# Optimization experiments

Hardware: AMD Instinct MI355X
Metric: run time of the kernel (lower is better)

The kernel has to match this reference:

```python
import jax, jax.numpy as jnp
import numpy as np

N_NODES = 50000
N_EDGES = 800000
NFEAT, NHID, NOUT = 128, 128, 64


def _glorot(key, shape):
    lim = 1.0 / np.sqrt(shape[0])
    return jax.random.uniform(key, shape, jnp.float32, -lim, lim)


def setup_inputs() -> dict:
    key = jax.random.key(0)
    ks = jax.random.split(key, 12)
    x = jax.random.normal(ks[0], (N_NODES, NFEAT), jnp.float32)
    edge_src = jax.random.randint(ks[1], (N_EDGES,), 0, N_NODES, jnp.int32)
    edge_dst = jax.random.randint(ks[2], (N_EDGES,), 0, N_NODES, jnp.int32)
    edge_w = jax.random.uniform(ks[3], (N_EDGES,), jnp.float32)  # normalized adj values
    # layer params: nfeat->nhid, nhid->nhid, nhid->nhid, nhid->nout
    W0, b0 = _glorot(ks[4], (NFEAT, NHID)), jnp.zeros((NHID,), jnp.float32)
    W1, b1 = _glorot(ks[5], (NHID, NHID)), jnp.zeros((NHID,), jnp.float32)
    W2, b2 = _glorot(ks[6], (NHID, NHID)), jnp.zeros((NHID,), jnp.float32)
    W3, b3 = _glorot(ks[7], (NHID, NOUT)), jnp.zeros((NOUT,), jnp.float32)
    return dict(x=x, edge_src=edge_src, edge_dst=edge_dst, edge_w=edge_w,
                W0=W0, b0=b0, W1=W1, b1=b1, W2=W2, b2=b2, W3=W3, b3=b3)


def _gcn_layer(h, src, dst, w, W, b):
    # support = h @ W ; out = A @ support + b  (A given as weighted edge list)
    support = h @ W                               # [N, d_out]
    msgs = support[src] * w[:, None]              # [E, d_out] gather + scale
    agg = jax.ops.segment_sum(msgs, dst, num_segments=N_NODES)  # scatter-add
    return agg + b


def reference(x, edge_src, edge_dst, edge_w, W0, b0, W1, b1, W2, b2, W3, b3):
    # eval mode: dropout is identity
    h = jax.nn.relu(_gcn_layer(x, edge_src, edge_dst, edge_w, W0, b0))
    h = jax.nn.relu(_gcn_layer(h, edge_src, edge_dst, edge_w, W1, b1))
    h = jax.nn.relu(_gcn_layer(h, edge_src, edge_dst, edge_w, W2, b2))
    h = _gcn_layer(h, edge_src, edge_dst, edge_w, W3, b3)  # no relu on last layer
    return h
```

## Files before the change

kernel.cpp:

```cpp
#include <hip/hip_runtime.h>


constexpr int NN = 50000;
constexpr int NE = 800000;
constexpr int NB = (NN + 127) >> 7;
constexpr int CAP = 4608;
constexpr int PART_CHUNK = 4096;
constexpr int PART_GRID = (NE + PART_CHUNK - 1) / PART_CHUNK;
constexpr int ZOFF = NB * CAP;

typedef __attribute__((ext_vector_type(8))) short bf16x8;
typedef __attribute__((ext_vector_type(4))) float floatx4;
typedef __attribute__((ext_vector_type(2))) float floatx2;
typedef __attribute__((ext_vector_type(4))) unsigned int uintx4;

__device__ inline unsigned short f2bf(float f) {
    unsigned u = __float_as_uint(f);
    u += 0x7fffu + ((u >> 16) & 1u);
    return (unsigned short)(u >> 16);
}
__device__ inline float bflo(unsigned v) { return __uint_as_float(v << 16); }
__device__ inline float bfhi(unsigned v) { return __uint_as_float(v & 0xffff0000u); }
__device__ inline unsigned char f2fp8(float f) {
    return (unsigned char)(__builtin_amdgcn_cvt_pk_fp8_f32(f, f, 0, false) & 0xff);
}


__global__ void k_prep(
        const float* __restrict__ W0, const float* __restrict__ W1,
        const float* __restrict__ W2, const float* __restrict__ W3,
        unsigned short* __restrict__ T0, unsigned short* __restrict__ T1,
        unsigned short* __restrict__ T2, unsigned short* __restrict__ T3,
        int* __restrict__ bfill, unsigned* __restrict__ es) {
    int b = blockIdx.x;
    if (b == 448) {
        for (int i = threadIdx.x; i < NB; i += 128) bfill[i] = 0;
        if (threadIdx.x < 16) es[ZOFF + threadIdx.x] = 0u;
        return;
    }
    const float* W; unsigned short* T; int N, n;
    if (b < 128)      { W = W0; T = T0; N = 128; n = b; }
    else if (b < 256) { W = W1; T = T1; N = 128; n = b - 128; }
    else if (b < 384) { W = W2; T = T2; N = 128; n = b - 256; }
    else              { W = W3; T = T3; N = 64;  n = b - 384; }
    int k = threadIdx.x;
    T[n * 128 + k] = f2bf(W[(size_t)k * N + n]);
}


__device__ inline bf16x8 ldA_f32(const float* A, size_t off) {
    float4 u = *(const float4*)&A[off];
    float4 v = *(const float4*)&A[off + 4];
    bf16x8 r;
    r[0] = (short)f2bf(u.x); r[1] = (short)f2bf(u.y);
    r[2] = (short)f2bf(u.z); r[3] = (short)f2bf(u.w);
    r[4] = (short)f2bf(v.x); r[5] = (short)f2bf(v.y);
    r[6] = (short)f2bf(v.z); r[7] = (short)f2bf(v.w);
    return r;
}

__global__ __launch_bounds__(256) void k_pg0(
        const int* __restrict__ src, const int* __restrict__ dst,
        const float* __restrict__ w, int* __restrict__ bfill,
        int2* __restrict__ ep,
        const float* __restrict__ A,
        const unsigned short* __restrict__ Wt,
        unsigned char* __restrict__ C,
        int M) {
    __shared__ int hist[NB], base[NB], off[NB];
    __shared__ unsigned short sWt[128 * 136];

    const int tid = threadIdx.x;

    if (blockIdx.x < PART_GRID) {
        for (int b = tid; b < NB; b += 256) { hist[b] = 0; off[b] = 0; }
        __syncthreads();

        int e0 = blockIdx.x * PART_CHUNK;
        int  sreg[16]; int wreg[16]; short breg[16];
#pragma unroll
        for (int i = 0; i < 16; ++i) {
            int e = e0 + i * 256 + tid;
            if (e < NE) {
                int d = dst[e];
                int b = d >> 7;
                sreg[i] = (src[e] & 0xffff) | ((d & 127) << 16);
                wreg[i] = __float_as_int(w[e]);
                breg[i] = (short)b;
                atomicAdd(&hist[b], 1);
            } else breg[i] = -1;
        }
        __syncthreads();
        for (int b = tid; b < NB; b += 256)
            base[b] = b * CAP + atomicAdd(&bfill[b], hist[b]);
        __syncthreads();
#pragma unroll
        for (int i = 0; i < 16; ++i) {
            if (breg[i] >= 0) {
                int b = breg[i];
                int p = atomicAdd(&off[b], 1);
                ep[base[b] + p] = make_int2(sreg[i], wreg[i]);
            }
        }
        return;
    }

    constexpr int STR = 136;
    const int gb = blockIdx.x - PART_GRID;
#pragma unroll
    for (int i = 0; i < 8; ++i) {
        int c = i * 256 + tid;
        int row = c >> 4, col = (c & 15) * 8;
        *(uint4*)&sWt[row * STR + col] = *(const uint4*)&Wt[row * 128 + col];
    }

    const int wv = tid >> 6;
    const int ln = tid & 63;
    const int m  = ln & 15;
    const int qd = ln >> 4;

    int gr  = gb * 64 + wv * 16 + m;
    int grc = (gr < M) ? gr : (M - 1);
    bf16x8 af[4];
#pragma unroll
    for (int s = 0; s < 4; ++s)
        af[s] = ldA_f32(A, (size_t)grc * 128 + s * 32 + qd * 8);

    __syncthreads();

    floatx4 acc[8];
#pragma unroll
    for (int c = 0; c < 8; ++c) {
        acc[c] = (floatx4){0.f, 0.f, 0.f, 0.f};
#pragma unroll
        for (int s = 0; s < 4; ++s) {
            bf16x8 bf = *(const bf16x8*)&sWt[(c * 16 + m) * STR + s * 32 + qd * 8];
            acc[c] = __builtin_amdgcn_mfma_f32_16x16x32_bf16(af[s], bf, acc[c], 0, 0, 0);
        }
    }

    int row0 = gb * 64 + wv * 16 + qd * 4;
#pragma unroll
    for (int c = 0; c < 8; ++c)
#pragma unroll
        for (int r = 0; r < 4; ++r) {
            int row = row0 + r;
            if (row < M) C[(size_t)row * 128 + c * 16 + m] = f2fp8(acc[c][r]);
        }
}

__global__ __launch_bounds__(256) void k_sort(
        const int2* __restrict__ ep, const int* __restrict__ bfill,
        unsigned* __restrict__ es, int2* __restrict__ begend) {
    __shared__ int cnt[128], base[128], fl[128];
    __shared__ int s_total;
    int b  = blockIdx.x;
    int n0 = b << 7;
    int nn = min(128, NN - n0);
    int t  = threadIdx.x;
    if (t < 128) { cnt[t] = 0; fl[t] = 0; }
    __syncthreads();
    int bbase = b * CAP;
    int beg = bbase, end = bbase + bfill[b];
    for (int e = beg + t; e < end; e += 256)
        atomicAdd(&cnt[(ep[e].x >> 16) & 127], 1);
    __syncthreads();
    int cp = (t < 128) ? ((cnt[t] + 15) & ~15) : 0;
    if (t < 128) base[t] = cp;
    __syncthreads();
    for (int off = 1; off < 128; off <<= 1) {
        int add = (t >= off && t < 128) ? base[t - off] : 0;
        __syncthreads();
        if (t < 128) base[t] += add;
        __syncthreads();
    }
    if (t == 127) s_total = base[127];
    __syncthreads();
    int total = s_total;
    for (int i = t; i < total + 16; i += 256) es[bbase + i] = 0u;
    if (t < nn) {
        int off = base[t] - cp;
        begend[n0 + t] = make_int2(bbase + off, bbase + off + cp);
    }
    __syncthreads();
    for (int e = beg + t; e < end; e += 256) {
        int2 v = ep[e];
        int d = (v.x >> 16) & 127;
        int off = base[d] - ((cnt[d] + 15) & ~15);
        int pos = bbase + off + atomicAdd(&fl[d], 1);
        es[pos] = (unsigned)(v.x & 0xffff) |
                  ((unsigned)f2bf(__int_as_float(v.y)) << 16);
    }
}


#define FMAP8(W, R)                                                             \
    { floatx2 p0 = __builtin_amdgcn_cvt_pk_f32_fp8((int)(R).x, false);          \
      floatx2 p1 = __builtin_amdgcn_cvt_pk_f32_fp8((int)(R).x, true);           \
      floatx2 p2 = __builtin_amdgcn_cvt_pk_f32_fp8((int)(R).y, false);          \
      floatx2 p3 = __builtin_amdgcn_cvt_pk_f32_fp8((int)(R).y, true);           \
      acc[0] = fmaf(W, p0.x, acc[0]); acc[1] = fmaf(W, p0.y, acc[1]);           \
      acc[2] = fmaf(W, p1.x, acc[2]); acc[3] = fmaf(W, p1.y, acc[3]);           \
      acc[4] = fmaf(W, p2.x, acc[4]); acc[5] = fmaf(W, p2.y, acc[5]);           \
      acc[6] = fmaf(W, p3.x, acc[6]); acc[7] = fmaf(W, p3.y, acc[7]); }

#define GATHF(R, MV)                                                            \
    uint2 R = *(const uint2*)&sup[(size_t)((MV) & 0xffffu) * 128 + l * 8];

template<int NOUT, typename CT>
__global__ __launch_bounds__(256) void k_fused(
        const unsigned char* __restrict__ sup,
        const int2* __restrict__ begend, const unsigned* __restrict__ es,
        const float* __restrict__ bias,
        const unsigned short* __restrict__ Wt,
        CT* __restrict__ C,
        int M) {
    constexpr int NT  = NOUT / 16;
    constexpr int STR = 136;
    __shared__ unsigned short hT[16 * STR];

    const int tid = threadIdx.x;
    const int l   = tid & 15;
    const int n0  = blockIdx.x * 16;
    const int n   = n0 + (tid >> 4);
    const bool nv = n < NN;

    int2 be = nv ? begend[n] : make_int2(0, 0);
    const int en = be.y;
    int e = be.x;
    float acc[8] = {0.f, 0.f, 0.f, 0.f, 0.f, 0.f, 0.f, 0.f};
    bool v = e < en;
    if (__any(v)) {
        int ei = v ? e : ZOFF;
        uintx4 m0 = __builtin_nontemporal_load((const uintx4*)&es[ei]);
        uintx4 m1 = __builtin_nontemporal_load((const uintx4*)&es[ei + 4]);
        for (;;) {
            GATHF(r0, m0[0]); GATHF(r1, m0[1]); GATHF(r2, m0[2]); GATHF(r3, m0[3]);
            GATHF(r4, m1[0]); GATHF(r5, m1[1]); GATHF(r6, m1[2]); GATHF(r7, m1[3]);
            float w0 = bfhi(m0[0]), w1 = bfhi(m0[1]), w2 = bfhi(m0[2]), w3 = bfhi(m0[3]);
            float w4 = bfhi(m1[0]), w5 = bfhi(m1[1]), w6 = bfhi(m1[2]), w7 = bfhi(m1[3]);
            e += 8;
            v = e < en;
            bool more = __any(v);
            int eo = v ? e : ZOFF;
            uintx4 p0 = __builtin_nontemporal_load((const uintx4*)&es[eo]);
            uintx4 p1 = __builtin_nontemporal_load((const uintx4*)&es[eo + 4]);
            FMAP8(w0, r0); FMAP8(w1, r1); FMAP8(w2, r2); FMAP8(w3, r3);
            FMAP8(w4, r4); FMAP8(w5, r5); FMAP8(w6, r6); FMAP8(w7, r7);
            m0 = p0; m1 = p1;
            if (!more) break;
        }
    }
    {
        uintx4 pk;
#pragma unroll
        for (int q = 0; q < 4; ++q) {
            float a0 = fmaxf(acc[2 * q]     + bias[l * 8 + 2 * q],     0.f);
            float a1 = fmaxf(acc[2 * q + 1] + bias[l * 8 + 2 * q + 1], 0.f);
            pk[q] = (unsigned)f2bf(a0) | ((unsigned)f2bf(a1) << 16);
        }
        *(uintx4*)&hT[(tid >> 4) * STR + l * 8] = pk;
    }
    __syncthreads();

    const int wv = tid >> 6;
    const int ln = tid & 63;
    const int m_ = ln & 15, qd = ln >> 4;
    const int c0 = wv * (NT / 4);
    bf16x8 af[4];
#pragma unroll
    for (int s = 0; s < 4; ++s)
        af[s] = *(const bf16x8*)&hT[m_ * STR + s * 32 + qd * 8];

    floatx4 acc2[NT / 4];
#pragma unroll
    for (int c = 0; c < NT / 4; ++c) {
        acc2[c] = (floatx4){0.f, 0.f, 0.f, 0.f};
#pragma unroll
        for (int s = 0; s < 4; ++s) {
            bf16x8 bf = *(const bf16x8*)&Wt[(size_t)((c0 + c) * 16 + m_) * 128 + s * 32 + qd * 8];
            acc2[c] = __builtin_amdgcn_mfma_f32_16x16x32_bf16(af[s], bf, acc2[c], 0, 0, 0);
        }
    }
    int row0 = n0 + qd * 4;
#pragma unroll
    for (int c = 0; c < NT / 4; ++c)
#pragma unroll
        for (int r = 0; r < 4; ++r) {
            int row = row0 + r;
            if (row < M) {
                if constexpr (sizeof(CT) == 1)
                    C[(size_t)row * NOUT + (c0 + c) * 16 + m_] = (CT)f2fp8(acc2[c][r]);
                else
                    C[(size_t)row * NOUT + (c0 + c) * 16 + m_] = (CT)f2bf(acc2[c][r]);
            }
        }
}


#define FMA4(W, R)                                                              \
    acc[0] = fmaf(W, bflo((R).x), acc[0]); acc[1] = fmaf(W, bfhi((R).x), acc[1]); \
    acc[2] = fmaf(W, bflo((R).y), acc[2]); acc[3] = fmaf(W, bfhi((R).y), acc[3]);

#define GATHO(R, MV)                                                            \
    uint2 R = *(const uint2*)&sup[(size_t)((MV) & 0xffffu) * 64 + l * 4];

__global__ __launch_bounds__(256) void k_agg64(
        const unsigned short* __restrict__ sup,
        const int2* __restrict__ begend, const unsigned* __restrict__ es,
        const float* __restrict__ bias, float* __restrict__ out) {
    const int tid = threadIdx.x;
    const int l   = tid & 15;
    const int n   = blockIdx.x * 16 + (tid >> 4);
    const bool nv = n < NN;

    int2 be = nv ? begend[n] : make_int2(0, 0);
    const int en = be.y;
    int e = be.x;
    float acc[4] = {0.f, 0.f, 0.f, 0.f};
    bool v = e < en;
    if (__any(v)) {
        int ei = v ? e : ZOFF;
        uintx4 m0 = __builtin_nontemporal_load((const uintx4*)&es[ei]);
        uintx4 m1 = __builtin_nontemporal_load((const uintx4*)&es[ei + 4]);
        for (;;) {
            GATHO(r0, m0[0]); GATHO(r1, m0[1]); GATHO(r2, m0[2]); GATHO(r3, m0[3]);
            GATHO(r4, m1[0]); GATHO(r5, m1[1]); GATHO(r6, m1[2]); GATHO(r7, m1[3]);
            float w0 = bfhi(m0[0]), w1 = bfhi(m0[1]), w2 = bfhi(m0[2]), w3 = bfhi(m0[3]);
            float w4 = bfhi(m1[0]), w5 = bfhi(m1[1]), w6 = bfhi(m1[2]), w7 = bfhi(m1[3]);
            e += 8;
            v = e < en;
            bool more = __any(v);
            int eo = v ? e : ZOFF;
            uintx4 p0 = __builtin_nontemporal_load((const uintx4*)&es[eo]);
            uintx4 p1 = __builtin_nontemporal_load((const uintx4*)&es[eo + 4]);
            FMA4(w0, r0); FMA4(w1, r1); FMA4(w2, r2); FMA4(w3, r3);
            FMA4(w4, r4); FMA4(w5, r5); FMA4(w6, r6); FMA4(w7, r7);
            m0 = p0; m1 = p1;
            if (!more) break;
        }
    }
    if (nv) {
        float4 o = make_float4(acc[0] + bias[l * 4],     acc[1] + bias[l * 4 + 1],
                               acc[2] + bias[l * 4 + 2], acc[3] + bias[l * 4 + 3]);
        *(float4*)&out[(size_t)n * 64 + l * 4] = o;
    }
}


extern "C" void kernel_launch(void* const* d_in, const int* in_sizes, int n_in,
                              void* d_out, int out_size, void* d_ws, size_t ws_size,
                              hipStream_t stream) {
    (void)in_sizes; (void)n_in; (void)out_size; (void)ws_size;

    const float* x    = (const float*)d_in[0];
    const int*   esrc = (const int*)d_in[1];
    const int*   edst = (const int*)d_in[2];
    const float* ew   = (const float*)d_in[3];
    const float* W0   = (const float*)d_in[4];
    const float* b0   = (const float*)d_in[5];
    const float* W1   = (const float*)d_in[6];
    const float* b1   = (const float*)d_in[7];
    const float* W2   = (const float*)d_in[8];
    const float* b2   = (const float*)d_in[9];
    const float* W3   = (const float*)d_in[10];
    const float* b3   = (const float*)d_in[11];

    char* p = (char*)d_ws;
    auto alloc = [&](size_t bytes) {
        char* r = p;
        p += (bytes + 511) & ~size_t(511);
        return r;
    };
    int*      bfill  = (int*)     alloc((size_t)NB * 4);
    int2*     begend = (int2*)    alloc((size_t)NN * 8);
    int2*     ep     = (int2*)    alloc((size_t)NB * CAP * 8);
    unsigned* es     = (unsigned*)alloc(((size_t)NB * CAP + 64) * 4);
    unsigned char*  s8a = (unsigned char*) alloc((size_t)NN * 128);
    unsigned char*  s8b = (unsigned char*) alloc((size_t)NN * 128);
    unsigned short* s16 = (unsigned short*)alloc((size_t)NN * 64 * 2);
    unsigned short* Wt0 = (unsigned short*)alloc((size_t)128 * 128 * 2);
    unsigned short* Wt1 = (unsigned short*)alloc((size_t)128 * 128 * 2);
    unsigned short* Wt2 = (unsigned short*)alloc((size_t)128 * 128 * 2);
    unsigned short* Wt3 = (unsigned short*)alloc((size_t)64 * 128 * 2);

    const int g_gemm = (NN + 63) / 64;
    const int f_grid = (NN + 15) / 16;

    k_prep<<<449, 128, 0, stream>>>(W0, W1, W2, W3, Wt0, Wt1, Wt2, Wt3,
                                    bfill, es);
    k_pg0<<<PART_GRID + g_gemm, 256, 0, stream>>>(
        esrc, edst, ew, bfill, ep, x, Wt0, s8a, NN);
    k_sort<<<NB, 256, 0, stream>>>(ep, bfill, es, begend);

    k_fused<128, unsigned char><<<f_grid, 256, 0, stream>>>(s8a, begend, es, b0, Wt1, s8b, NN);
    k_fused<128, unsigned char><<<f_grid, 256, 0, stream>>>(s8b, begend, es, b1, Wt2, s8a, NN);
    k_fused<64, unsigned short><<<f_grid, 256, 0, stream>>>(s8a, begend, es, b2, Wt3, s16, NN);
    k_agg64<<<f_grid, 256, 0, stream>>>(s16, begend, es, b3, (float*)d_out);
}
```

Before: 233.6 us.

## Merge weight prep with edge partition and sort with first GEMM

Restructures the preprocessing pipeline. The weight transpose/convert work is folded into the edge-partition kernel. The per-bucket sort is folded into the same launch as the first-layer GEMM. The zeroing of bfill and the es tail moves to hipMemsetAsync calls. This cuts kernel launches from three to two plus two memsets, and lets the sort and GEMM work overlap in one grid, at the cost of shared-memory aliasing between roles and two extra memset operations.

```diff
diff --git a/kernel.cpp b/kernel.cpp
--- a/kernel.cpp
+++ b/kernel.cpp
@@ -8,6 +8,7 @@
 constexpr int PART_CHUNK = 4096;
 constexpr int PART_GRID = (NE + PART_CHUNK - 1) / PART_CHUNK;
 constexpr int ZOFF = NB * CAP;
+constexpr int PREP_GRID = 224;
 
 typedef __attribute__((ext_vector_type(8))) short bf16x8;
 typedef __attribute__((ext_vector_type(4))) float floatx4;
@@ -26,25 +27,58 @@
 }
 
 
-__global__ void k_prep(
+__global__ __launch_bounds__(256) void k_pp(
         const float* __restrict__ W0, const float* __restrict__ W1,
         const float* __restrict__ W2, const float* __restrict__ W3,
         unsigned short* __restrict__ T0, unsigned short* __restrict__ T1,
         unsigned short* __restrict__ T2, unsigned short* __restrict__ T3,
-        int* __restrict__ bfill, unsigned* __restrict__ es) {
-    int b = blockIdx.x;
-    if (b == 448) {
-        for (int i = threadIdx.x; i < NB; i += 128) bfill[i] = 0;
-        if (threadIdx.x < 16) es[ZOFF + threadIdx.x] = 0u;
+        const int* __restrict__ src, const int* __restrict__ dst,
+        const float* __restrict__ w, int* __restrict__ bfill,
+        int2* __restrict__ ep) {
+    const int tid = threadIdx.x;
+
+    if (blockIdx.x < PREP_GRID) {
+        int r = blockIdx.x * 2 + (tid >> 7);
+        int k = tid & 127;
+        const float* W; unsigned short* T; int N, n;
+        if (r < 128)      { W = W0; T = T0; N = 128; n = r; }
+        else if (r < 256) { W = W1; T = T1; N = 128; n = r - 128; }
+        else if (r < 384) { W = W2; T = T2; N = 128; n = r - 256; }
+        else              { W = W3; T = T3; N = 64;  n = r - 384; }
+        T[n * 128 + k] = f2bf(W[(size_t)k * N + n]);
         return;
     }
-    const float* W; unsigned short* T; int N, n;
-    if (b < 128)      { W = W0; T = T0; N = 128; n = b; }
-    else if (b < 256) { W = W1; T = T1; N = 128; n = b - 128; }
-    else if (b < 384) { W = W2; T = T2; N = 128; n = b - 256; }
-    else              { W = W3; T = T3; N = 64;  n = b - 384; }
-    int k = threadIdx.x;
-    T[n * 128 + k] = f2bf(W[(size_t)k * N + n]);
+
+    __shared__ int hist[NB], base[NB], off[NB];
+    for (int b = tid; b < NB; b += 256) { hist[b] = 0; off[b] = 0; }
+    __syncthreads();
+
+    int e0 = (blockIdx.x - PREP_GRID) * PART_CHUNK;
+    int  sreg[16]; int wreg[16]; short breg[16];
+#pragma unroll
+    for (int i = 0; i < 16; ++i) {
+        int e = e0 + i * 256 + tid;
+        if (e < NE) {
+            int d = dst[e];
+            int b = d >> 7;
+            sreg[i] = (src[e] & 0xffff) | ((d & 127) << 16);
+            wreg[i] = __float_as_int(w[e]);
+            breg[i] = (short)b;
+            atomicAdd(&hist[b], 1);
+        } else breg[i] = -1;
+    }
+    __syncthreads();
+    for (int b = tid; b < NB; b += 256)
+        base[b] = b * CAP + atomicAdd(&bfill[b], hist[b]);
+    __syncthreads();
+#pragma unroll
+    for (int i = 0; i < 16; ++i) {
+        if (breg[i] >= 0) {
+            int b = breg[i];
+            int p = atomicAdd(&off[b], 1);
+            ep[base[b] + p] = make_int2(sreg[i], wreg[i]);
+        }
+    }
 }
 
 
@@ -59,54 +93,64 @@
     return r;
 }
 
-__global__ __launch_bounds__(256) void k_pg0(
-        const int* __restrict__ src, const int* __restrict__ dst,
-        const float* __restrict__ w, int* __restrict__ bfill,
-        int2* __restrict__ ep,
+__global__ __launch_bounds__(256) void k_sg(
+        const int2* __restrict__ ep, const int* __restrict__ bfill,
+        unsigned* __restrict__ es, int2* __restrict__ begend,
         const float* __restrict__ A,
         const unsigned short* __restrict__ Wt,
         unsigned char* __restrict__ C,
         int M) {
-    __shared__ int hist[NB], base[NB], off[NB];
-    __shared__ unsigned short sWt[128 * 136];
-
+    constexpr int STR = 136;
+    __shared__ int smem[128 * STR / 2];
     const int tid = threadIdx.x;
 
-    if (blockIdx.x < PART_GRID) {
-        for (int b = tid; b < NB; b += 256) { hist[b] = 0; off[b] = 0; }
+    if (blockIdx.x < NB) {
+        int* cnt  = smem;
+        int* base = smem + 128;
+        int* fl   = smem + 256;
+        int* stot = smem + 384;
+        int b  = blockIdx.x;
+        int n0 = b << 7;
+        int nn = min(128, NN - n0);
+        int t  = tid;
+        if (t < 128) { cnt[t] = 0; fl[t] = 0; }
         __syncthreads();
-
-        int e0 = blockIdx.x * PART_CHUNK;
-        int  sreg[16]; int wreg[16]; short breg[16];
-#pragma unroll
-        for (int i = 0; i < 16; ++i) {
-            int e = e0 + i * 256 + tid;
-            if (e < NE) {
-                int d = dst[e];
-                int b = d >> 7;
-                sreg[i] = (src[e] & 0xffff) | ((d & 127) << 16);
-                wreg[i] = __float_as_int(w[e]);
-                breg[i] = (short)b;
-                atomicAdd(&hist[b], 1);
-            } else breg[i] = -1;
-        }
+        int bbase = b * CAP;
+        int beg = bbase, end = bbase + bfill[b];
+        for (int e = beg + t; e < end; e += 256)
+            atomicAdd(&cnt[(ep[e].x >> 16) & 127], 1);
         __syncthreads();
-        for (int b = tid; b < NB; b += 256)
-            base[b] = b * CAP + atomicAdd(&bfill[b], hist[b]);
+        int cp = (t < 128) ? ((cnt[t] + 15) & ~15) : 0;
+        if (t < 128) base[t] = cp;
         __syncthreads();
-#pragma unroll
-        for (int i = 0; i < 16; ++i) {
-            if (breg[i] >= 0) {
-                int b = breg[i];
-                int p = atomicAdd(&off[b], 1);
-                ep[base[b] + p] = make_int2(sreg[i], wreg[i]);
-            }
+        for (int off = 1; off < 128; off <<= 1) {
+            int add = (t >= off && t < 128) ? base[t - off] : 0;
+            __syncthreads();
+            if (t < 128) base[t] += add;
+            __syncthreads();
+        }
+        if (t == 127) *stot = base[127];
+        __syncthreads();
+        int total = *stot;
+        for (int i = t; i < total + 16; i += 256) es[bbase + i] = 0u;
+        if (t < nn) {
+            int off = base[t] - cp;
+            begend[n0 + t] = make_int2(bbase + off, bbase + off + cp);
+        }
+        __syncthreads();
+        for (int e = beg + t; e < end; e += 256) {
+            int2 v = ep[e];
+            int d = (v.x >> 16) & 127;
+            int off = base[d] - ((cnt[d] + 15) & ~15);
+            int pos = bbase + off + atomicAdd(&fl[d], 1);
+            es[pos] = (unsigned)(v.x & 0xffff) |
+                      ((unsigned)f2bf(__int_as_float(v.y)) << 16);
         }
         return;
     }
 
-    constexpr int STR = 136;
-    const int gb = blockIdx.x - PART_GRID;
+    unsigned short* sWt = (unsigned short*)smem;
+    const int gb = blockIdx.x - NB;
 #pragma unroll
     for (int i = 0; i < 8; ++i) {
         int c = i * 256 + tid;
@@ -147,50 +191,6 @@
             int row = row0 + r;
             if (row < M) C[(size_t)row * 128 + c * 16 + m] = f2fp8(acc[c][r]);
         }
-}
-
-__global__ __launch_bounds__(256) void k_sort(
-        const int2* __restrict__ ep, const int* __restrict__ bfill,
-        unsigned* __restrict__ es, int2* __restrict__ begend) {
-    __shared__ int cnt[128], base[128], fl[128];
-    __shared__ int s_total;
-    int b  = blockIdx.x;
-    int n0 = b << 7;
-    int nn = min(128, NN - n0);
-    int t  = threadIdx.x;
-    if (t < 128) { cnt[t] = 0; fl[t] = 0; }
-    __syncthreads();
-    int bbase = b * CAP;
-    int beg = bbase, end = bbase + bfill[b];
-    for (int e = beg + t; e < end; e += 256)
-        atomicAdd(&cnt[(ep[e].x >> 16) & 127], 1);
-    __syncthreads();
-    int cp = (t < 128) ? ((cnt[t] + 15) & ~15) : 0;
-    if (t < 128) base[t] = cp;
-    __syncthreads();
-    for (int off = 1; off < 128; off <<= 1) {
-        int add = (t >= off && t < 128) ? base[t - off] : 0;
-        __syncthreads();
-        if (t < 128) base[t] += add;
-        __syncthreads();
-    }
-    if (t == 127) s_total = base[127];
-    __syncthreads();
-    int total = s_total;
-    for (int i = t; i < total + 16; i += 256) es[bbase + i] = 0u;
-    if (t < nn) {
-        int off = base[t] - cp;
-        begend[n0 + t] = make_int2(bbase + off, bbase + off + cp);
-    }
-    __syncthreads();
-    for (int e = beg + t; e < end; e += 256) {
-        int2 v = ep[e];
-        int d = (v.x >> 16) & 127;
-        int off = base[d] - ((cnt[d] + 15) & ~15);
-        int pos = bbase + off + atomicAdd(&fl[d], 1);
-        es[pos] = (unsigned)(v.x & 0xffff) |
-                  ((unsigned)f2bf(__int_as_float(v.y)) << 16);
-    }
 }
 
 
@@ -387,11 +387,12 @@
     const int g_gemm = (NN + 63) / 64;
     const int f_grid = (NN + 15) / 16;
 
-    k_prep<<<449, 128, 0, stream>>>(W0, W1, W2, W3, Wt0, Wt1, Wt2, Wt3,
-                                    bfill, es);
-    k_pg0<<<PART_GRID + g_gemm, 256, 0, stream>>>(
-        esrc, edst, ew, bfill, ep, x, Wt0, s8a, NN);
-    k_sort<<<NB, 256, 0, stream>>>(ep, bfill, es, begend);
+    hipMemsetAsync(bfill, 0, (size_t)NB * 4, stream);
+    hipMemsetAsync(es + ZOFF, 0, 16 * 4, stream);
+    k_pp<<<PREP_GRID + PART_GRID, 256, 0, stream>>>(
+        W0, W1, W2, W3, Wt0, Wt1, Wt2, Wt3, esrc, edst, ew, bfill, ep);
+    k_sg<<<NB + g_gemm, 256, 0, stream>>>(
+        ep, bfill, es, begend, x, Wt0, s8a, NN);
 
     k_fused<128, unsigned char><<<f_grid, 256, 0, stream>>>(s8a, begend, es, b0, Wt1, s8b, NN);
     k_fused<128, unsigned char><<<f_grid, 256, 0, stream>>>(s8b, begend, es, b1, Wt2, s8a, NN);
```

Result: slower. 238.7 us (+2.2%).
